# Optimization experiments

Measured on AMD Instinct MI355X. Metric: run time of the kernel, lower is better.

The kernel has to match this reference:

```python
import jax, jax.numpy as jnp
import numpy as np

H = 8        # heads
DH = 64      # dim_head
EPS = 1e-5   # LayerNorm eps (torch default)


def setup_inputs() -> dict:
    key = jax.random.key(0)
    k0, k1, k2, k3, k4 = jax.random.split(key, 5)
    b, l, n, dim = 2, 8, 256, 512
    inner = H * DH
    return {
        "xyzs": jax.random.normal(k0, (b, l, n, 3), dtype=jnp.float32),
        "features": jax.random.normal(k1, (b, l, n, dim), dtype=jnp.float32),
        "ln_gamma": jnp.ones((dim,), dtype=jnp.float32),
        "ln_beta": jnp.zeros((dim,), dtype=jnp.float32),
        "w_qkv": jax.random.normal(k2, (dim, 3 * inner), dtype=jnp.float32) * 0.02,
        "w_sp": jax.random.normal(k3, (3, DH), dtype=jnp.float32) * 0.3,
        "w_out": jax.random.normal(k4, (inner, dim), dtype=jnp.float32) * 0.02,
        "b_out": jnp.zeros((dim,), dtype=jnp.float32),
    }


def reference(xyzs, features, ln_gamma, ln_beta, w_qkv, w_sp, w_out, b_out):
    b, l, n, dim = features.shape
    m = l * n
    inner = H * DH
    scale = DH ** (-0.5)

    # LayerNorm over last dim (biased variance, eps=1e-5)
    mu = jnp.mean(features, axis=-1, keepdims=True)
    var = jnp.var(features, axis=-1, keepdims=True)
    normed = (features - mu) * jax.lax.rsqrt(var + EPS) * ln_gamma + ln_beta

    # qkv projection, chunk into q,k,v, reshape 'b l n (h d) -> b h (l n) d'
    qkv = normed.reshape(b, m, dim) @ w_qkv            # [b, m, 3*inner]
    def split_heads(t):
        return t.reshape(b, m, H, DH).transpose(0, 2, 1, 3)  # [b, h, m, d]
    q = split_heads(qkv[..., :inner])
    k = split_heads(qkv[..., inner:2 * inner])
    v = split_heads(qkv[..., 2 * inner:])

    dots = jnp.einsum('bhid,bhjd->bhij', q, k) * scale  # [b, h, m, m]
    attn = jax.nn.softmax(dots, axis=-1)
    v_out = jnp.einsum('bhij,bhjd->bhid', attn, v)      # [b, h, m, d]

    # pairwise coordinate deltas: delta[b,i,j,c] = xyz[b,j,c] - xyz[b,i,c]
    xyz_f = xyzs.reshape(b, m, 3)
    delta = xyz_f[:, None, :, :] - xyz_f[:, :, None, :]  # [b, m, m, 3]
    # attention-weighted aggregation over j (avoids [b,h,m,m,3] intermediate)
    agg = jnp.einsum('bhij,bijc->bhic', attn, delta)     # [b, h, m, 3]
    disp = agg @ w_sp                                    # [b, h, m, DH]

    out = v_out + disp                                   # [b, h, m, DH]
    out = out.transpose(0, 2, 1, 3).reshape(b, m, inner) # 'b h m d -> b m (h d)'
    out = jax.nn.gelu(out @ w_out + b_out, approximate=False)
    return out.reshape(b, l, n, dim) + features
```

## Files before the change

kernel.cpp:

```cpp
#include <hip/hip_runtime.h>
#include <hip/hip_bf16.h>
#include <math.h>

#define BB   2
#define MM   2048
#define DIM  512
#define NH   8
#define DHd  64
#define NQK  1536
#define ROWS 4096
#define NROW 32768
#define SPLITK 4

typedef __hip_bfloat16 bf16;
typedef __attribute__((ext_vector_type(8))) short bf16x8;
typedef __attribute__((ext_vector_type(4))) float f32x4;
typedef __attribute__((ext_vector_type(16))) float f32x16;
typedef __attribute__((ext_vector_type(8))) unsigned short us8;
typedef __attribute__((ext_vector_type(4))) unsigned int u32x4;

__device__ __forceinline__ unsigned short f2bf_bits(float x) {
    bf16 h = __float2bfloat16(x);
    return *(unsigned short*)&h;
}
__device__ __forceinline__ float bf2f(unsigned short u) {
    unsigned int v = ((unsigned int)u) << 16;
    return __uint_as_float(v);
}
__device__ __forceinline__ unsigned cvtpk_bf16(float lo, float hi) {
    unsigned r;
    asm("v_cvt_pk_bf16_f32 %0, %1, %2" : "=v"(r) : "v"(lo), "v"(hi));
    return r;
}
__device__ __forceinline__ void pl32swap(unsigned &a, unsigned &b) {
    asm volatile("v_permlane32_swap_b32 %0, %1" : "+v"(a), "+v"(b));
}

__global__ __launch_bounds__(256) void pre_kernel(
    const float* __restrict__ feat, const float* __restrict__ gamma,
    const float* __restrict__ beta, unsigned short* __restrict__ normed,
    const float* __restrict__ wqkv, const float* __restrict__ wout,
    unsigned short* __restrict__ wqkvT, unsigned short* __restrict__ woutT)
{
    __shared__ float st[64][65];
    int b = blockIdx.x;
    int tid = threadIdx.x;
    if (b < ROWS / 4) {
        int w = tid >> 6, lane = tid & 63;
        int row = b * 4 + w;
        const float* fr = feat + (size_t)row * DIM + lane * 8;
        float4 v0 = *(const float4*)fr;
        float4 v1 = *(const float4*)(fr + 4);
        float s  = v0.x + v0.y + v0.z + v0.w + v1.x + v1.y + v1.z + v1.w;
        float ss = v0.x*v0.x + v0.y*v0.y + v0.z*v0.z + v0.w*v0.w
                 + v1.x*v1.x + v1.y*v1.y + v1.z*v1.z + v1.w*v1.w;
        #pragma unroll
        for (int o = 32; o >= 1; o >>= 1) { s += __shfl_xor(s, o); ss += __shfl_xor(ss, o); }
        float mu  = s * (1.0f / DIM);
        float var = ss * (1.0f / DIM) - mu * mu;
        float inv = rsqrtf(var + 1e-5f);
        const float* gp = gamma + lane * 8;
        const float* bp = beta  + lane * 8;
        float4 g0 = *(const float4*)gp, g1 = *(const float4*)(gp + 4);
        float4 e0 = *(const float4*)bp, e1 = *(const float4*)(bp + 4);
        unsigned short ov[8];
        ov[0] = f2bf_bits((v0.x - mu) * inv * g0.x + e0.x);
        ov[1] = f2bf_bits((v0.y - mu) * inv * g0.y + e0.y);
        ov[2] = f2bf_bits((v0.z - mu) * inv * g0.z + e0.z);
        ov[3] = f2bf_bits((v0.w - mu) * inv * g0.w + e0.w);
        ov[4] = f2bf_bits((v1.x - mu) * inv * g1.x + e1.x);
        ov[5] = f2bf_bits((v1.y - mu) * inv * g1.y + e1.y);
        ov[6] = f2bf_bits((v1.z - mu) * inv * g1.z + e1.z);
        ov[7] = f2bf_bits((v1.w - mu) * inv * g1.w + e1.w);
        *(us8*)&normed[(size_t)row * DIM + lane * 8] = *(us8*)ov;
        return;
    }
    int idx = b - ROWS / 4;
    const float* in; unsigned short* out; int N, n0;
    if (idx < 192) { in = wqkv; out = wqkvT; N = NQK; n0 = (idx >> 3) * 64; }
    else { idx -= 192; in = wout; out = woutT; N = DIM; n0 = (idx >> 3) * 64; }
    int k0 = (idx & 7) * 64;
    #pragma unroll
    for (int p = 0; p < 16; p++) {
        int e = tid + p * 256;
        int r = e >> 6, c = e & 63;
        st[r][c] = in[(size_t)(k0 + r) * N + n0 + c];
    }
    __syncthreads();
    #pragma unroll
    for (int p = 0; p < 16; p++) {
        int e = tid + p * 256;
        int nr = e >> 6, kc = e & 63;
        out[(size_t)(n0 + nr) * DIM + k0 + kc] = f2bf_bits(st[kc][nr]);
    }
}

__global__ __launch_bounds__(256) void qkv_gemm(
    const unsigned short* __restrict__ A, const unsigned short* __restrict__ BT,
    unsigned short* __restrict__ qd, unsigned short* __restrict__ kd,
    unsigned short* __restrict__ vd)
{
    __shared__ __align__(16) unsigned short sA[128 * 72];
    __shared__ __align__(16) unsigned short sB[64 * 72];
    int tid = threadIdx.x;
    int r0 = blockIdx.x * 128;
    int n0 = blockIdx.y * 64;
    int chunk = n0 >> 9;
    int h     = (n0 & 511) >> 6;
    int w = tid >> 6, lane = tid & 63;
    int wm = w >> 1, wn = w & 1;
    int ln15 = lane & 15, quad = lane >> 4;

    int arow = tid >> 1, acol = (tid & 1) * 32;
    int brow = tid >> 2, bcol = (tid & 3) * 16;

    f32x4 acc[4][2] = {};
    us8 ra[4], rb[2];

    #pragma unroll
    for (int u = 0; u < 4; u++)
        ra[u] = *(const us8*)&A[(size_t)(r0 + arow) * DIM + acol + u * 8];
    #pragma unroll
    for (int u = 0; u < 2; u++)
        rb[u] = *(const us8*)&BT[(size_t)(n0 + brow) * DIM + bcol + u * 8];

    for (int k0 = 0; k0 < DIM; k0 += 64) {
        __syncthreads();
        #pragma unroll
        for (int u = 0; u < 4; u++) *(us8*)&sA[arow * 72 + acol + u * 8] = ra[u];
        #pragma unroll
        for (int u = 0; u < 2; u++) *(us8*)&sB[brow * 72 + bcol + u * 8] = rb[u];
        __syncthreads();
        int kn = k0 + 64;
        if (kn < DIM) {
            #pragma unroll
            for (int u = 0; u < 4; u++)
                ra[u] = *(const us8*)&A[(size_t)(r0 + arow) * DIM + kn + acol + u * 8];
            #pragma unroll
            for (int u = 0; u < 2; u++)
                rb[u] = *(const us8*)&BT[(size_t)(n0 + brow) * DIM + kn + bcol + u * 8];
        }
        bf16x8 fa[4][2], fb[2][2];
        #pragma unroll
        for (int i = 0; i < 4; i++)
            #pragma unroll
            for (int kk = 0; kk < 2; kk++)
                fa[i][kk] = *(const bf16x8*)&sA[(wm * 64 + i * 16 + ln15) * 72 + kk * 32 + quad * 8];
        #pragma unroll
        for (int j = 0; j < 2; j++)
            #pragma unroll
            for (int kk = 0; kk < 2; kk++)
                fb[j][kk] = *(const bf16x8*)&sB[(wn * 32 + j * 16 + ln15) * 72 + kk * 32 + quad * 8];
        if (chunk == 2) {
            #pragma unroll
            for (int kk = 0; kk < 2; kk++)
                #pragma unroll
                for (int i = 0; i < 4; i++)
                    #pragma unroll
                    for (int j = 0; j < 2; j++)
                        acc[i][j] = __builtin_amdgcn_mfma_f32_16x16x32_bf16(fa[i][kk], fb[j][kk], acc[i][j], 0, 0, 0);
        } else {
            #pragma unroll
            for (int kk = 0; kk < 2; kk++)
                #pragma unroll
                for (int i = 0; i < 4; i++)
                    #pragma unroll
                    for (int j = 0; j < 2; j++)
                        acc[i][j] = __builtin_amdgcn_mfma_f32_16x16x32_bf16(fb[j][kk], fa[i][kk], acc[i][j], 0, 0, 0);
        }
    }

    if (chunk == 2) {
        #pragma unroll
        for (int i = 0; i < 4; i++) {
            int gm = r0 + wm * 64 + i * 16 + quad * 4;
            int bb = gm >> 11, mm = gm & 2047;
            #pragma unroll
            for (int j = 0; j < 2; j++) {
                int d = wn * 32 + j * 16 + ln15;
                ushort4 pk;
                pk.x = f2bf_bits(acc[i][j][0]);
                pk.y = f2bf_bits(acc[i][j][1]);
                pk.z = f2bf_bits(acc[i][j][2]);
                pk.w = f2bf_bits(acc[i][j][3]);
                *(ushort4*)&vd[((size_t)(bb * NH + h) * DHd + d) * MM + mm] = pk;
            }
        }
    } else {
        unsigned short* dst = (chunk == 0) ? qd : kd;
        float sc = (chunk == 0) ? 0.18033688f : 1.0f;
        #pragma unroll
        for (int i = 0; i < 4; i++) {
            int gm = r0 + wm * 64 + i * 16 + ln15;
            int bb = gm >> 11, mm = gm & 2047;
            #pragma unroll
            for (int j = 0; j < 2; j++) {
                int d0 = wn * 32 + j * 16 + quad * 4;
                ushort4 pk;
                pk.x = f2bf_bits(acc[i][j][0] * sc);
                pk.y = f2bf_bits(acc[i][j][1] * sc);
                pk.z = f2bf_bits(acc[i][j][2] * sc);
                pk.w = f2bf_bits(acc[i][j][3] * sc);
                *(ushort4*)&dst[((size_t)(bb * NH + h) * MM + mm) * DHd + d0] = pk;
            }
        }
    }
}

__global__ __launch_bounds__(256, 4) void attn_kernel(
    const unsigned short* __restrict__ qg, const unsigned short* __restrict__ kg,
    const unsigned short* __restrict__ vg, const float* __restrict__ xyzs,
    unsigned short* __restrict__ obuf, float* __restrict__ lbuf)
{
    __shared__ __align__(16) unsigned short sK[64 * 72];
    __shared__ __align__(16) unsigned short sVT[96 * 72];

    int tid = threadIdx.x;
    int bh = blockIdx.y; int bb = bh >> 3;
    int i0 = blockIdx.x * 128;
    int ks = blockIdx.z;
    int wid = tid >> 6;
    int lane = tid & 63;
    int ln31 = lane & 31;
    int hi   = lane >> 5;
    int hi8  = hi * 8;

    for (int e = tid; e < 28 * 72; e += 256) sVT[68 * 72 + e] = 0;
    if (tid < 64) sVT[67 * 72 + tid] = 0x3F80;

    bf16x8 aq[4];
    {
        const unsigned short* q0 = qg + ((size_t)bh * MM + i0 + wid * 32 + ln31) * DHd + hi8;
        #pragma unroll
        for (int kc = 0; kc < 4; kc++)
            aq[kc] = *(const bf16x8*)(q0 + kc * 16);
    }

    f32x16 ot[3] = {};

    const unsigned short* kbase = kg + (size_t)bh * MM * DHd;
    const unsigned short* vbase = vg + (size_t)bh * DHd * MM;
    int jbeg = ks * (MM / SPLITK);

    int srow = tid >> 2, scolB = (tid & 3) * 16;
    int key0 = tid / 3, c0 = tid - key0 * 3;

    us8 rk0, rk1, rv0, rv1;
    float rx = 0.f;
    {
        const unsigned short* ksrc = kbase + (size_t)(jbeg + srow) * DHd + scolB;
        const unsigned short* vsrc = vbase + (size_t)srow * MM + jbeg + scolB;
        rk0 = *(const us8*)ksrc;
        rk1 = *(const us8*)(ksrc + 8);
        rv0 = *(const us8*)vsrc;
        rv1 = *(const us8*)(vsrc + 8);
        if (tid < 192) rx = xyzs[((size_t)bb * MM + jbeg) * 3 + tid];
    }

    for (int t = 0; t < MM / SPLITK / 64; ++t) {
        int jt = jbeg + t * 64;
        __syncthreads();
        *(us8*)&sK[srow * 72 + scolB]      = rk0;
        *(us8*)&sK[srow * 72 + scolB + 8]  = rk1;
        *(us8*)&sVT[srow * 72 + scolB]     = rv0;
        *(us8*)&sVT[srow * 72 + scolB + 8] = rv1;
        if (tid < 192) sVT[(64 + c0) * 72 + key0] = f2bf_bits(rx);
        __syncthreads();
        int jn = jt + 64;
        if (jn < jbeg + MM / SPLITK) {
            const unsigned short* ksrc = kbase + (size_t)(jn + srow) * DHd + scolB;
            const unsigned short* vsrc = vbase + (size_t)srow * MM + jn + scolB;
            rk0 = *(const us8*)ksrc;
            rk1 = *(const us8*)(ksrc + 8);
            rv0 = *(const us8*)vsrc;
            rv1 = *(const us8*)(vsrc + 8);
            if (tid < 192) rx = xyzs[((size_t)bb * MM + jn) * 3 + tid];
        }

        #pragma unroll
        for (int b = 0; b < 2; b++) {
            f32x16 zz = {};
            #pragma unroll
            for (int kc = 0; kc < 4; kc++) {
                bf16x8 kf = *(const bf16x8*)&sK[(b * 32 + ln31) * 72 + kc * 16 + hi8];
                zz = __builtin_amdgcn_mfma_f32_32x32x16_bf16(kf, aq[kc], zz, 0, 0, 0);
            }
            unsigned c_[8];
            #pragma unroll
            for (int j = 0; j < 8; j++)
                c_[j] = cvtpk_bf16(exp2f(zz[2 * j]), exp2f(zz[2 * j + 1]));
            unsigned x0 = c_[0], x2 = c_[2]; pl32swap(x0, x2);
            unsigned x1 = c_[1], x3 = c_[3]; pl32swap(x1, x3);
            unsigned y0 = c_[4], y2 = c_[6]; pl32swap(y0, y2);
            unsigned y1 = c_[5], y3 = c_[7]; pl32swap(y1, y3);
            u32x4 xv = {x0, x1, x2, x3};
            u32x4 yv = {y0, y1, y2, y3};
            bf16x8 X = *(bf16x8*)&xv;
            bf16x8 Y = *(bf16x8*)&yv;
            #pragma unroll
            for (int vb = 0; vb < 3; vb++) {
                bf16x8 v0 = *(const bf16x8*)&sVT[(vb * 32 + ln31) * 72 + b * 32 + hi8];
                bf16x8 v1 = *(const bf16x8*)&sVT[(vb * 32 + ln31) * 72 + b * 32 + 16 + hi8];
                ot[vb] = __builtin_amdgcn_mfma_f32_32x32x16_bf16(v0, X, ot[vb], 0, 0, 0);
                ot[vb] = __builtin_amdgcn_mfma_f32_32x32x16_bf16(v1, Y, ot[vb], 0, 0, 0);
            }
        }
    }

    size_t kso = (size_t)ks * NROW;
    size_t row = (size_t)bh * MM + i0 + wid * 32 + ln31;
    unsigned short* orow = obuf + (kso + row) * 72;
    #pragma unroll
    for (int vb = 0; vb < 2; vb++) {
        #pragma unroll
        for (int rq = 0; rq < 4; rq++) {
            ushort4 pk;
            pk.x = f2bf_bits(ot[vb][rq * 4 + 0]);
            pk.y = f2bf_bits(ot[vb][rq * 4 + 1]);
            pk.z = f2bf_bits(ot[vb][rq * 4 + 2]);
            pk.w = f2bf_bits(ot[vb][rq * 4 + 3]);
            *(ushort4*)&orow[vb * 32 + rq * 8 + hi * 4] = pk;
        }
    }
    if (hi == 0) {
        orow[64] = f2bf_bits(ot[2][0]);
        orow[65] = f2bf_bits(ot[2][1]);
        orow[66] = f2bf_bits(ot[2][2]);
        lbuf[kso + row] = ot[2][3];
    }
}

__global__ __launch_bounds__(256) void merge_kernel(
    const unsigned short* __restrict__ obuf, const float* __restrict__ lbuf,
    const float* __restrict__ xyzs, const float* __restrict__ wsp,
    unsigned short* __restrict__ attn_out)
{
    __shared__ float sW[3][64];
    int tid = threadIdx.x;
    if (tid < 192) sW[tid >> 6][tid & 63] = wsp[tid];
    __syncthreads();
    int r   = blockIdx.x * 64 + (tid >> 2);
    int d0  = (tid & 3) * 16;
    int bh = r >> 11, qrow = r & 2047, bb = bh >> 3, hh = bh & 7;
    const unsigned short* p0 = obuf + (size_t)r * 72;
    const unsigned short* p1 = p0 + (size_t)NROW * 72;
    const unsigned short* p2 = p1 + (size_t)NROW * 72;
    const unsigned short* p3 = p2 + (size_t)NROW * 72;
    float invl = 1.f / (lbuf[r] + lbuf[NROW + r] + lbuf[2 * NROW + r] + lbuf[3 * NROW + r]);
    size_t xb = ((size_t)bb * MM + qrow) * 3;
    float gx = (bf2f(p0[64]) + bf2f(p1[64]) + bf2f(p2[64]) + bf2f(p3[64])) * invl - xyzs[xb + 0];
    float gy = (bf2f(p0[65]) + bf2f(p1[65]) + bf2f(p2[65]) + bf2f(p3[65])) * invl - xyzs[xb + 1];
    float gz = (bf2f(p0[66]) + bf2f(p1[66]) + bf2f(p2[66]) + bf2f(p3[66])) * invl - xyzs[xb + 2];
    us8 a0 = *(const us8*)&p0[d0];
    us8 a1 = *(const us8*)&p0[d0 + 8];
    us8 b0 = *(const us8*)&p1[d0];
    us8 b1 = *(const us8*)&p1[d0 + 8];
    us8 c0 = *(const us8*)&p2[d0];
    us8 c1 = *(const us8*)&p2[d0 + 8];
    us8 e0 = *(const us8*)&p3[d0];
    us8 e1 = *(const us8*)&p3[d0 + 8];
    unsigned short outv[16];
    #pragma unroll
    for (int e = 0; e < 8; e++) {
        int d = d0 + e;
        float v = (bf2f(a0[e]) + bf2f(b0[e]) + bf2f(c0[e]) + bf2f(e0[e])) * invl
                + gx * sW[0][d] + gy * sW[1][d] + gz * sW[2][d];
        outv[e] = f2bf_bits(v);
    }
    #pragma unroll
    for (int e = 0; e < 8; e++) {
        int d = d0 + 8 + e;
        float v = (bf2f(a1[e]) + bf2f(b1[e]) + bf2f(c1[e]) + bf2f(e1[e])) * invl
                + gx * sW[0][d] + gy * sW[1][d] + gz * sW[2][d];
        outv[8 + e] = f2bf_bits(v);
    }
    unsigned short* dst = attn_out + ((size_t)bb * MM + qrow) * DIM + hh * DHd + d0;
    *(us8*)dst       = *(us8*)&outv[0];
    *(us8*)(dst + 8) = *(us8*)&outv[8];
}

__global__ __launch_bounds__(256) void out_gemm(
    const unsigned short* __restrict__ A, const unsigned short* __restrict__ BT,
    const float* __restrict__ bias, const float* __restrict__ feat,
    float* __restrict__ out)
{
    __shared__ __align__(16) unsigned short sA[64 * 72];
    __shared__ __align__(16) unsigned short sB[64 * 72];
    int tid = threadIdx.x;
    int r0 = blockIdx.x * 64, n0 = blockIdx.y * 64;
    int w = tid >> 6, lane = tid & 63;
    int wm = w >> 1, wn = w & 1;
    int ln15 = lane & 15, quad = lane >> 4;

    int srow = tid >> 2, scol = (tid & 3) * 16;

    f32x4 acc[2][2] = {};
    us8 ra[2], rb[2];

    #pragma unroll
    for (int u = 0; u < 2; u++) {
        ra[u] = *(const us8*)&A[(size_t)(r0 + srow) * DIM + scol + u * 8];
        rb[u] = *(const us8*)&BT[(size_t)(n0 + srow) * DIM + scol + u * 8];
    }

    for (int k0 = 0; k0 < DIM; k0 += 64) {
        __syncthreads();
        #pragma unroll
        for (int u = 0; u < 2; u++) {
            *(us8*)&sA[srow * 72 + scol + u * 8] = ra[u];
            *(us8*)&sB[srow * 72 + scol + u * 8] = rb[u];
        }
        __syncthreads();
        int kn = k0 + 64;
        if (kn < DIM) {
            #pragma unroll
            for (int u = 0; u < 2; u++) {
                ra[u] = *(const us8*)&A[(size_t)(r0 + srow) * DIM + kn + scol + u * 8];
                rb[u] = *(const us8*)&BT[(size_t)(n0 + srow) * DIM + kn + scol + u * 8];
            }
        }
        bf16x8 af[2][2], bf_[2][2];
        #pragma unroll
        for (int i = 0; i < 2; i++)
            #pragma unroll
            for (int kk = 0; kk < 2; kk++)
                af[i][kk] = *(const bf16x8*)&sA[(wm * 32 + i * 16 + ln15) * 72 + kk * 32 + quad * 8];
        #pragma unroll
        for (int j = 0; j < 2; j++)
            #pragma unroll
            for (int kk = 0; kk < 2; kk++)
                bf_[j][kk] = *(const bf16x8*)&sB[(wn * 32 + j * 16 + ln15) * 72 + kk * 32 + quad * 8];
        #pragma unroll
        for (int kk = 0; kk < 2; kk++)
            #pragma unroll
            for (int i = 0; i < 2; i++)
                #pragma unroll
                for (int j = 0; j < 2; j++)
                    acc[i][j] = __builtin_amdgcn_mfma_f32_16x16x32_bf16(af[i][kk], bf_[j][kk], acc[i][j], 0, 0, 0);
    }

    #pragma unroll
    for (int i = 0; i < 2; i++) {
        #pragma unroll
        for (int reg = 0; reg < 4; reg++) {
            int gr = r0 + wm * 32 + i * 16 + quad * 4 + reg;
            #pragma unroll
            for (int j = 0; j < 2; j++) {
                int c = n0 + wn * 32 + j * 16 + ln15;
                float x = acc[i][j][reg] + bias[c];
                float g = 0.5f * x * (1.f + erff(x * 0.70710678118f));
                out[(size_t)gr * DIM + c] = g + feat[(size_t)gr * DIM + c];
            }
        }
    }
}

extern "C" void kernel_launch(void* const* d_in, const int* in_sizes, int n_in,
                              void* d_out, int out_size, void* d_ws, size_t ws_size,
                              hipStream_t stream)
{
    const float* xyzs  = (const float*)d_in[0];
    const float* feat  = (const float*)d_in[1];
    const float* gamma = (const float*)d_in[2];
    const float* beta  = (const float*)d_in[3];
    const float* wqkv  = (const float*)d_in[4];
    const float* wsp   = (const float*)d_in[5];
    const float* wout  = (const float*)d_in[6];
    const float* bout  = (const float*)d_in[7];
    float* out = (float*)d_out;

    unsigned short* ws16 = (unsigned short*)d_ws;
    const size_t SEGS = (size_t)ROWS * DIM;
    unsigned short* normed = ws16;
    unsigned short* qb     = ws16 + SEGS;
    unsigned short* kb     = ws16 + 2 * SEGS;
    unsigned short* vb     = ws16 + 3 * SEGS;
    unsigned short* wqkvT  = ws16 + 4 * SEGS;
    unsigned short* woutT  = wqkvT + (size_t)NQK * DIM;
    unsigned short* obuf   = woutT + (size_t)DIM * DIM;
    float*          lbuf   = (float*)(obuf + (size_t)SPLITK * NROW * 72);

    pre_kernel<<<ROWS / 4 + 256, 256, 0, stream>>>(feat, gamma, beta, normed,
                                                   wqkv, wout, wqkvT, woutT);
    qkv_gemm<<<dim3(32, 24), 256, 0, stream>>>(normed, wqkvT, qb, kb, vb);
    attn_kernel<<<dim3(16, 16, SPLITK), 256, 0, stream>>>(qb, kb, vb, xyzs, obuf, lbuf);
    merge_kernel<<<512, 256, 0, stream>>>(obuf, lbuf, xyzs, wsp, normed);
    out_gemm<<<dim3(64, 8), 256, 0, stream>>>(normed, woutT, bout, feat, out);
}
```

Before: 143.1 us.

## Process two query fragments per warp in attention to reuse K/V tiles

Each warp now computes 64 query rows as two 32-row fragments, sharing each K and V LDS fragment load across both. The block covers 256 queries, so the grid halves and K/V global loads per query halve. Launch bounds drop to 2 blocks per CU to make room for the doubled accumulators and Q registers. In exchange, occupancy and block count fall, which may hurt latency hiding.

```diff
diff --git a/kernel.cpp b/kernel.cpp
--- a/kernel.cpp
+++ b/kernel.cpp
@@ -207,7 +207,7 @@
     }
 }
 
-__global__ __launch_bounds__(256, 4) void attn_kernel(
+__global__ __launch_bounds__(256, 2) void attn_kernel(
     const unsigned short* __restrict__ qg, const unsigned short* __restrict__ kg,
     const unsigned short* __restrict__ vg, const float* __restrict__ xyzs,
     unsigned short* __restrict__ obuf, float* __restrict__ lbuf)
@@ -217,7 +217,7 @@
 
     int tid = threadIdx.x;
     int bh = blockIdx.y; int bb = bh >> 3;
-    int i0 = blockIdx.x * 128;
+    int i0 = blockIdx.x * 256;
     int ks = blockIdx.z;
     int wid = tid >> 6;
     int lane = tid & 63;
@@ -228,15 +228,16 @@
     for (int e = tid; e < 28 * 72; e += 256) sVT[68 * 72 + e] = 0;
     if (tid < 64) sVT[67 * 72 + tid] = 0x3F80;
 
-    bf16x8 aq[4];
-    {
-        const unsigned short* q0 = qg + ((size_t)bh * MM + i0 + wid * 32 + ln31) * DHd + hi8;
+    bf16x8 aq[2][4];
+    #pragma unroll
+    for (int qf = 0; qf < 2; qf++) {
+        const unsigned short* q0 = qg + ((size_t)bh * MM + i0 + wid * 64 + qf * 32 + ln31) * DHd + hi8;
         #pragma unroll
         for (int kc = 0; kc < 4; kc++)
-            aq[kc] = *(const bf16x8*)(q0 + kc * 16);
-    }
-
-    f32x16 ot[3] = {};
+            aq[qf][kc] = *(const bf16x8*)(q0 + kc * 16);
+    }
+
+    f32x16 ot[2][3] = {};
 
     const unsigned short* kbase = kg + (size_t)bh * MM * DHd;
     const unsigned short* vbase = vg + (size_t)bh * DHd * MM;
@@ -279,54 +280,66 @@
 
         #pragma unroll
         for (int b = 0; b < 2; b++) {
-            f32x16 zz = {};
-            #pragma unroll
-            for (int kc = 0; kc < 4; kc++) {
-                bf16x8 kf = *(const bf16x8*)&sK[(b * 32 + ln31) * 72 + kc * 16 + hi8];
-                zz = __builtin_amdgcn_mfma_f32_32x32x16_bf16(kf, aq[kc], zz, 0, 0, 0);
-            }
-            unsigned c_[8];
-            #pragma unroll
-            for (int j = 0; j < 8; j++)
-                c_[j] = cvtpk_bf16(exp2f(zz[2 * j]), exp2f(zz[2 * j + 1]));
-            unsigned x0 = c_[0], x2 = c_[2]; pl32swap(x0, x2);
-            unsigned x1 = c_[1], x3 = c_[3]; pl32swap(x1, x3);
-            unsigned y0 = c_[4], y2 = c_[6]; pl32swap(y0, y2);
-            unsigned y1 = c_[5], y3 = c_[7]; pl32swap(y1, y3);
-            u32x4 xv = {x0, x1, x2, x3};
-            u32x4 yv = {y0, y1, y2, y3};
-            bf16x8 X = *(bf16x8*)&xv;
-            bf16x8 Y = *(bf16x8*)&yv;
+            bf16x8 kf[4];
+            #pragma unroll
+            for (int kc = 0; kc < 4; kc++)
+                kf[kc] = *(const bf16x8*)&sK[(b * 32 + ln31) * 72 + kc * 16 + hi8];
+            bf16x8 X[2], Y[2];
+            #pragma unroll
+            for (int qf = 0; qf < 2; qf++) {
+                f32x16 zz = {};
+                #pragma unroll
+                for (int kc = 0; kc < 4; kc++)
+                    zz = __builtin_amdgcn_mfma_f32_32x32x16_bf16(kf[kc], aq[qf][kc], zz, 0, 0, 0);
+                unsigned c_[8];
+                #pragma unroll
+                for (int j = 0; j < 8; j++)
+                    c_[j] = cvtpk_bf16(exp2f(zz[2 * j]), exp2f(zz[2 * j + 1]));
+                unsigned x0 = c_[0], x2 = c_[2]; pl32swap(x0, x2);
+                unsigned x1 = c_[1], x3 = c_[3]; pl32swap(x1, x3);
+                unsigned y0 = c_[4], y2 = c_[6]; pl32swap(y0, y2);
+                unsigned y1 = c_[5], y3 = c_[7]; pl32swap(y1, y3);
+                u32x4 xv = {x0, x1, x2, x3};
+                u32x4 yv = {y0, y1, y2, y3};
+                X[qf] = *(bf16x8*)&xv;
+                Y[qf] = *(bf16x8*)&yv;
+            }
             #pragma unroll
             for (int vb = 0; vb < 3; vb++) {
                 bf16x8 v0 = *(const bf16x8*)&sVT[(vb * 32 + ln31) * 72 + b * 32 + hi8];
                 bf16x8 v1 = *(const bf16x8*)&sVT[(vb * 32 + ln31) * 72 + b * 32 + 16 + hi8];
-                ot[vb] = __builtin_amdgcn_mfma_f32_32x32x16_bf16(v0, X, ot[vb], 0, 0, 0);
-                ot[vb] = __builtin_amdgcn_mfma_f32_32x32x16_bf16(v1, Y, ot[vb], 0, 0, 0);
+                #pragma unroll
+                for (int qf = 0; qf < 2; qf++) {
+                    ot[qf][vb] = __builtin_amdgcn_mfma_f32_32x32x16_bf16(v0, X[qf], ot[qf][vb], 0, 0, 0);
+                    ot[qf][vb] = __builtin_amdgcn_mfma_f32_32x32x16_bf16(v1, Y[qf], ot[qf][vb], 0, 0, 0);
+                }
             }
         }
     }
 
     size_t kso = (size_t)ks * NROW;
-    size_t row = (size_t)bh * MM + i0 + wid * 32 + ln31;
-    unsigned short* orow = obuf + (kso + row) * 72;
-    #pragma unroll
-    for (int vb = 0; vb < 2; vb++) {
-        #pragma unroll
-        for (int rq = 0; rq < 4; rq++) {
-            ushort4 pk;
-            pk.x = f2bf_bits(ot[vb][rq * 4 + 0]);
-            pk.y = f2bf_bits(ot[vb][rq * 4 + 1]);
-            pk.z = f2bf_bits(ot[vb][rq * 4 + 2]);
-            pk.w = f2bf_bits(ot[vb][rq * 4 + 3]);
-            *(ushort4*)&orow[vb * 32 + rq * 8 + hi * 4] = pk;
-        }
-    }
-    if (hi == 0) {
-        orow[64] = f2bf_bits(ot[2][0]);
-        orow[65] = f2bf_bits(ot[2][1]);
-        orow[66] = f2bf_bits(ot[2][2]);
-        lbuf[kso + row] = ot[2][3];
+    #pragma unroll
+    for (int qf = 0; qf < 2; qf++) {
+        size_t row = (size_t)bh * MM + i0 + wid * 64 + qf * 32 + ln31;
+        unsigned short* orow = obuf + (kso + row) * 72;
+        #pragma unroll
+        for (int vb = 0; vb < 2; vb++) {
+            #pragma unroll
+            for (int rq = 0; rq < 4; rq++) {
+                ushort4 pk;
+                pk.x = f2bf_bits(ot[qf][vb][rq * 4 + 0]);
+                pk.y = f2bf_bits(ot[qf][vb][rq * 4 + 1]);
+                pk.z = f2bf_bits(ot[qf][vb][rq * 4 + 2]);
+                pk.w = f2bf_bits(ot[qf][vb][rq * 4 + 3]);
+                *(ushort4*)&orow[vb * 32 + rq * 8 + hi * 4] = pk;
+            }
+        }
+        if (hi == 0) {
+            orow[64] = f2bf_bits(ot[qf][2][0]);
+            orow[65] = f2bf_bits(ot[qf][2][1]);
+            orow[66] = f2bf_bits(ot[qf][2][2]);
+            lbuf[kso + row] = ot[qf][2][3];
+        }
     }
 }
 
@@ -483,7 +496,7 @@
     pre_kernel<<<ROWS / 4 + 256, 256, 0, stream>>>(feat, gamma, beta, normed,
                                                    wqkv, wout, wqkvT, woutT);
     qkv_gemm<<<dim3(32, 24), 256, 0, stream>>>(normed, wqkvT, qb, kb, vb);
-    attn_kernel<<<dim3(16, 16, SPLITK), 256, 0, stream>>>(qb, kb, vb, xyzs, obuf, lbuf);
+    attn_kernel<<<dim3(8, 16, SPLITK), 256, 0, stream>>>(qb, kb, vb, xyzs, obuf, lbuf);
     merge_kernel<<<512, 256, 0, stream>>>(obuf, lbuf, xyzs, wsp, normed);
     out_gemm<<<dim3(64, 8), 256, 0, stream>>>(normed, woutT, bout, feat, out);
 }
```

After: 144.5 us. About the same (+1.0%).
